# Performance work log

Hardware: AMD Instinct MI355X
Metric: run time of the kernel (lower is better)

Reference implementation:

```python
import jax, jax.numpy as jnp
import numpy as np

E, QE, P, H = 3, 60000, 40, 20   # elements, atoms per element, fp length, hidden
NIMG = 1800                       # images in batch
Q = E * QE                        # total atoms
NNZ = 14_400_000                  # nnz of sparse fprimes [P*Q, 3*Q]


def setup_inputs() -> dict:
    key = jax.random.key(0)
    ks = jax.random.split(key, 12)
    fps = jax.random.normal(ks[0], (E, QE, P), jnp.float32)
    image_idx = jax.random.randint(ks[1], (E, QE), 0, NIMG, jnp.int32)
    s1 = 1.0 / np.sqrt(P)
    s2 = 1.0 / np.sqrt(H)
    W1 = (jax.random.normal(ks[2], (E, P, H)) * s1).astype(jnp.float32)
    b1 = jnp.zeros((E, H), jnp.float32)
    W2 = (jax.random.normal(ks[3], (E, H, H)) * s2).astype(jnp.float32)
    b2 = jnp.zeros((E, H), jnp.float32)
    W3 = (jax.random.normal(ks[4], (E, H, 1)) * s2).astype(jnp.float32)
    b3 = jnp.zeros((E, 1), jnp.float32)
    fp_rows = jax.random.randint(ks[5], (NNZ,), 0, P * Q, jnp.int32)
    fp_cols = jax.random.randint(ks[6], (NNZ,), 0, 3 * Q, jnp.int32)
    fp_vals = (jax.random.normal(ks[7], (NNZ,)) * 0.05).astype(jnp.float32)
    return {"fps": fps, "W1": W1, "b1": b1, "W2": W2, "b2": b2, "W3": W3,
            "b3": b3, "image_idx": image_idx, "fp_rows": fp_rows,
            "fp_cols": fp_cols, "fp_vals": fp_vals, "batch_size": NIMG}


def _mlp(x, w1, b1, w2, b2, w3, b3):
    # Dense(tanh) -> Dense(tanh) -> Dense(linear), per amptorch MLP(n_layers=3)
    h = jnp.tanh(x @ w1 + b1)
    h = jnp.tanh(h @ w2 + b2)
    return h @ w3 + b3  # [..., 1]


def _esum(x, w1, b1, w2, b2, w3, b3):
    return _mlp(x, w1, b1, w2, b2, w3, b3).sum()


def reference(fps, W1, b1, W2, b2, W3, b3, image_idx, fp_rows, fp_cols,
              fp_vals, batch_size):
    # per-element atomwise energies: [E, QE, 1]
    atom_e = jax.vmap(_mlp)(fps, W1, b1, W2, b2, W3, b3)
    # scatter-add atomic energies into per-image energies (index_add_)
    energy_pred = jax.ops.segment_sum(
        atom_e.reshape(-1, 1), image_idx.reshape(-1).astype(jnp.int32),
        num_segments=batch_size)  # [NIMG, 1]
    # dE/dFP per atom (each atom's output depends only on its own fp, so
    # grad of the per-element energy sum == per-atom jacobian rows)
    dE_dFP = jax.vmap(jax.grad(_esum))(fps, W1, b1, W2, b2, W3, b3)  # [E,QE,P]
    # reorder atoms from element-grouped order to image-index order
    # (stable argsort == boolean-match reorder in the torch code)
    order = jnp.argsort(image_idx.reshape(-1))
    dE_flat = dE_dFP.reshape(-1, P)[order].reshape(-1)  # [P*Q]
    # force = -fprimes^T @ dE_dFP  (sparse COO matvec via segment_sum)
    force_flat = -jax.ops.segment_sum(
        fp_vals * dE_flat[fp_rows], fp_cols, num_segments=3 * Q)
    force_pred = force_flat.reshape(-1, 3)  # [Q, 3]
    return energy_pred, force_pred
```

## Files before the change

kernel.cpp:

```cpp
#include <hip/hip_runtime.h>
#include <math.h>

#define E_    3
#define QE_   60000
#define QTOT  180000
#define P_    40
#define H_    20
#define NIMG_ 1800
#define NNZ_  14400000
#define BLK   256
#define NB    704

#define CW_BITS 12
#define CW      4096
#define NBIN    132
#define SUBS    8
#define SC      8192
#define NSB     1758

#define SLICE_SHIFT 17
#define NSLICE  55
#define CAPS    270336
#define CAPB    114688
#define MAXCH4  1815
#define FS_GRID 768
#define FS_PERX 96

#define C_SCUR  0
#define C_BCUR  64
#define C_GCNT  256
#define C_CHS   512
#define C_CHST  2432
#define C_CHLEN 4352
#define C_GRP   6272
#define C_INTS  8320

typedef int   vi4 __attribute__((ext_vector_type(4)));
typedef float vf4 __attribute__((ext_vector_type(4)));
typedef unsigned uint32;

__global__ void zero_kernel(float* __restrict__ out, int n) {
    int i = blockIdx.x * blockDim.x + threadIdx.x;
    if (i < n) out[i] = 0.0f;
}
__global__ void zero_ctrl_kernel(int* __restrict__ ctrl) {
    ctrl[threadIdx.x] = 0;
}

__global__ void hist_kernel(const int* __restrict__ img, int* __restrict__ g_hist) {
    __shared__ int h[NIMG_];
    const int t = threadIdx.x, b = blockIdx.x;
    for (int v = t; v < NIMG_; v += BLK) h[v] = 0;
    __syncthreads();
    int a = b * BLK + t;
    if (a < QTOT) atomicAdd(&h[img[a]], 1);
    __syncthreads();
    for (int v = t; v < NIMG_; v += BLK) g_hist[v * NB + b] = h[v];
}

__global__ void scan_blocks_kernel(int* __restrict__ g_hist, int* __restrict__ g_total) {
    __shared__ int s[BLK];
    const int v = blockIdx.x, t = threadIdx.x;
    int carry = 0;
    for (int c = 0; c < NB; c += BLK) {
        int idx = c + t;
        int val = (idx < NB) ? g_hist[v * NB + idx] : 0;
        s[t] = val; __syncthreads();
        for (int off = 1; off < BLK; off <<= 1) {
            int tmp = (t >= off) ? s[t - off] : 0;
            __syncthreads();
            s[t] += tmp;
            __syncthreads();
        }
        int excl = s[t] - val;
        int tot  = s[BLK - 1];
        if (idx < NB) g_hist[v * NB + idx] = carry + excl;
        carry += tot;
        __syncthreads();
    }
    if (t == 0) g_total[v] = carry;
}

__global__ void scan_buckets_kernel(const int* __restrict__ g_total, int* __restrict__ g_base) {
    __shared__ int s[BLK];
    const int t = threadIdx.x;
    int carry = 0;
    for (int c = 0; c < NIMG_; c += BLK) {
        int idx = c + t;
        int val = (idx < NIMG_) ? g_total[idx] : 0;
        s[t] = val; __syncthreads();
        for (int off = 1; off < BLK; off <<= 1) {
            int tmp = (t >= off) ? s[t - off] : 0;
            __syncthreads();
            s[t] += tmp;
            __syncthreads();
        }
        if (idx < NIMG_) g_base[idx] = carry + (s[t] - val);
        carry += s[BLK - 1];
        __syncthreads();
    }
}

__global__ void rank_kernel(const int* __restrict__ img, const int* __restrict__ g_hist,
                            const int* __restrict__ g_base, int* __restrict__ rank) {
    __shared__ int simg[BLK];
    const int t = threadIdx.x, b = blockIdx.x;
    int a = b * BLK + t;
    int v = (a < QTOT) ? img[a] : -1;
    simg[t] = v;
    __syncthreads();
    if (a < QTOT) {
        int local = 0;
        for (int j = 0; j < t; ++j) {
            if (simg[j] == v) local++;
        }
        rank[a] = g_base[v] + g_hist[v * NB + b] + local;
    }
}

__global__ __launch_bounds__(BLK) void mlp_kernel(
    const float* __restrict__ fps, const float* __restrict__ W1, const float* __restrict__ b1,
    const float* __restrict__ W2, const float* __restrict__ b2, const float* __restrict__ W3,
    const float* __restrict__ b3, const int* __restrict__ img, const int* __restrict__ rank,
    float* __restrict__ energy, float* __restrict__ dEflat)
{
    __shared__ float sW1[P_ * H_], sW2[H_ * H_], sW3[H_], sB1[H_], sB2[H_];
    __shared__ float sB3;
    const int e = blockIdx.y;
    const int t = threadIdx.x;
    for (int i = t; i < P_ * H_; i += BLK) sW1[i] = W1[e * P_ * H_ + i];
    for (int i = t; i < H_ * H_; i += BLK) sW2[i] = W2[e * H_ * H_ + i];
    if (t < H_) { sW3[t] = W3[e * H_ + t]; sB1[t] = b1[e * H_ + t]; sB2[t] = b2[e * H_ + t]; }
    if (t == 0) sB3 = b3[e];
    __syncthreads();

    int q = blockIdx.x * BLK + t;
    if (q >= QE_) return;
    int a = e * QE_ + q;

    const vf4* xp = (const vf4*)(fps + (size_t)a * P_);
    float x[P_];
    #pragma unroll
    for (int p = 0; p < P_; p += 4) {
        vf4 v4 = __builtin_nontemporal_load(xp + (p >> 2));
        x[p] = v4.x; x[p+1] = v4.y; x[p+2] = v4.z; x[p+3] = v4.w;
    }

    float h1v[H_], h2v[H_];
    #pragma unroll
    for (int i = 0; i < H_; ++i) {
        float z = sB1[i];
        #pragma unroll
        for (int p = 0; p < P_; ++p) z += x[p] * sW1[p * H_ + i];
        h1v[i] = tanhf(z);
    }
    #pragma unroll
    for (int i = 0; i < H_; ++i) {
        float z = sB2[i];
        #pragma unroll
        for (int j = 0; j < H_; ++j) z += h1v[j] * sW2[j * H_ + i];
        h2v[i] = tanhf(z);
    }
    float ea = sB3;
    #pragma unroll
    for (int i = 0; i < H_; ++i) ea += h2v[i] * sW3[i];
    atomicAdd(&energy[img[a]], ea);

    float dz2[H_];
    #pragma unroll
    for (int i = 0; i < H_; ++i) dz2[i] = sW3[i] * (1.0f - h2v[i] * h2v[i]);
    float dz1[H_];
    #pragma unroll
    for (int i = 0; i < H_; ++i) {
        float d = 0.0f;
        #pragma unroll
        for (int j = 0; j < H_; ++j) d += sW2[i * H_ + j] * dz2[j];
        dz1[i] = d * (1.0f - h1v[i] * h1v[i]);
    }
    float* op = dEflat + (size_t)rank[a] * P_;
    #pragma unroll
    for (int p = 0; p < P_; p += 4) {
        float4 v4;
        float d0 = 0.f, d1 = 0.f, d2 = 0.f, d3 = 0.f;
        #pragma unroll
        for (int i = 0; i < H_; ++i) {
            d0 += sW1[(p    ) * H_ + i] * dz1[i];
            d1 += sW1[(p + 1) * H_ + i] * dz1[i];
            d2 += sW1[(p + 2) * H_ + i] * dz1[i];
            d3 += sW1[(p + 3) * H_ + i] * dz1[i];
        }
        v4.x = d0; v4.y = d1; v4.z = d2; v4.w = d3;
        *(float4*)(op + p) = v4;
    }
}


__global__ __launch_bounds__(BLK) void slice_scatter_kernel(
    const int* __restrict__ rows, const int* __restrict__ cols, const float* __restrict__ vals,
    int* __restrict__ ctrl, uint2* __restrict__ items)
{
    __shared__ uint32 srow[SC];
    __shared__ int h[NSLICE], lcur[NSLICE], gbase[NSLICE];
    const int t = threadIdx.x, b = blockIdx.x;
    const int base = b * SC;
    const int len = min(SC, NNZ_ - base);
    const bool full = (len == SC);

    if (t < NSLICE) h[t] = 0;
    __syncthreads();
    if (full) {
        const vi4* r4 = (const vi4*)(rows + base);
        #pragma unroll
        for (int j = 0; j < SC / (BLK * 4); ++j) {
            int idx = j * BLK + t;
            vi4 rr = __builtin_nontemporal_load(r4 + idx);
            srow[idx * 4 + 0] = (uint32)rr.x; atomicAdd(&h[rr.x >> SLICE_SHIFT], 1);
            srow[idx * 4 + 1] = (uint32)rr.y; atomicAdd(&h[rr.y >> SLICE_SHIFT], 1);
            srow[idx * 4 + 2] = (uint32)rr.z; atomicAdd(&h[rr.z >> SLICE_SHIFT], 1);
            srow[idx * 4 + 3] = (uint32)rr.w; atomicAdd(&h[rr.w >> SLICE_SHIFT], 1);
        }
    } else {
        for (int j = t; j < len; j += BLK) {
            int r = rows[base + j];
            srow[j] = (uint32)r;
            atomicAdd(&h[r >> SLICE_SHIFT], 1);
        }
    }
    __syncthreads();
    if (t < NSLICE) {
        lcur[t] = 0;
        gbase[t] = (h[t] > 0) ? atomicAdd(&ctrl[C_SCUR + t], h[t]) : 0;
    }
    __syncthreads();
    if (full) {
        const vi4* c4 = (const vi4*)(cols + base);
        const vi4* v4 = (const vf4*)(vals + base) ? (const vi4*)(vals + base) : nullptr;
        #pragma unroll 2
        for (int j = 0; j < SC / (BLK * 4); ++j) {
            int idx = j * BLK + t;
            vi4 cc = __builtin_nontemporal_load(c4 + idx);
            vi4 vv = __builtin_nontemporal_load(v4 + idx);
            #define EMIT(K, CI, VB)                                                \
            {                                                                      \
                uint32 r = srow[idx * 4 + K];                                      \
                int sl = (int)(r >> SLICE_SHIFT);                                  \
                int pos = gbase[sl] + atomicAdd(&lcur[sl], 1);                     \
                uint32 v15 = (((uint32)(VB)) + 0x10000u) >> 17;                    \
                items[(size_t)sl * CAPS + pos] =                                   \
                    make_uint2((v15 << 17) | (r & 0x1FFFFu), (uint32)(CI));        \
            }
            EMIT(0, cc.x, vv.x)
            EMIT(1, cc.y, vv.y)
            EMIT(2, cc.z, vv.z)
            EMIT(3, cc.w, vv.w)
        }
    } else {
        for (int j = t; j < len; j += BLK) {
            uint32 r = srow[j];
            int sl = (int)(r >> SLICE_SHIFT);
            int pos = gbase[sl] + atomicAdd(&lcur[sl], 1);
            uint32 vb = ((const uint32*)vals)[base + j];
            uint32 v15 = (vb + 0x10000u) >> 17;
            items[(size_t)sl * CAPS + pos] =
                make_uint2((v15 << 17) | (r & 0x1FFFFu), (uint32)cols[base + j]);
        }
    }
}

__global__ void plan4_kernel(int* __restrict__ ctrl) {
    __shared__ int scnt[NSLICE], cb[NSLICE + 1], gp[NSLICE];
    __shared__ int g8[8], tot_s;
    const int t = threadIdx.x;
    if (t < NSLICE) scnt[t] = ctrl[C_SCUR + t];
    __syncthreads();
    if (t == 0) {
        int crun = 0;
        int gs[8]; for (int x = 0; x < 8; ++x) gs[x] = 0;
        for (int s = 0; s < NSLICE; ++s) {
            int nc = (scnt[s] + SC - 1) / SC;
            cb[s] = crun; crun += nc;
            int x = s & 7;
            gp[s] = gs[x]; gs[x] += nc;
        }
        cb[NSLICE] = crun; tot_s = crun;
        for (int x = 0; x < 8; ++x) g8[x] = gs[x];
    }
    __syncthreads();
    const int tot = tot_s;
    if (t < 8) ctrl[C_GCNT + t] = g8[t];
    for (int idx = t; idx < tot; idx += BLK) {
        int s = 0;
        for (int k = 0; k < NSLICE; ++k) if (cb[k] <= idx) s = k;
        int c = idx - cb[s];
        ctrl[C_CHS + idx]   = s;
        ctrl[C_CHST + idx]  = s * CAPS + c * SC;
        ctrl[C_CHLEN + idx] = min(SC, scnt[s] - c * SC);
        ctrl[C_GRP + (s & 7) * 256 + gp[s] + c] = idx;
    }
}

__global__ __launch_bounds__(BLK) void fscatter4_kernel(
    const uint2* __restrict__ items, const float* __restrict__ dEflat,
    int* __restrict__ ctrl, uint32* __restrict__ bm)
{
    __shared__ uint32 itl[SC];
    __shared__ unsigned char bns[SC];
    __shared__ int h[NBIN], cur[NBIN], dlt[NBIN];
    __shared__ int sc[BLK];
    const int t = threadIdx.x;
    const int x = blockIdx.x & 7;
    const int r = blockIdx.x >> 3;
    const int gc = ctrl[C_GCNT + x];

    for (int w = r; w < gc; w += FS_PERX) {
        const int g     = ctrl[C_GRP + x * 256 + w];
        const int sl    = ctrl[C_CHS + g];
        const int start = ctrl[C_CHST + g];
        const int len   = ctrl[C_CHLEN + g];
        const int row0  = sl << SLICE_SHIFT;
        const int lenE  = len & ~1;

        if (t < NBIN) h[t] = 0;
        __syncthreads();
        if (len == SC) {
            const vi4* p4 = (const vi4*)(items + start);
            #pragma unroll
            for (int j = 0; j < SC / (BLK * 2); ++j) {
                vi4 q = __builtin_nontemporal_load(p4 + j * BLK + t);
                atomicAdd(&h[((uint32)q.y) >> CW_BITS], 1);
                atomicAdd(&h[((uint32)q.w) >> CW_BITS], 1);
            }
        } else {
            for (int j = t; j < len; j += BLK)
                atomicAdd(&h[items[start + j].y >> CW_BITS], 1);
        }
        __syncthreads();
        {
            int v = (t < NBIN) ? h[t] : 0;
            sc[t] = v; __syncthreads();
            for (int off = 1; off < BLK; off <<= 1) {
                int tmp = (t >= off) ? sc[t - off] : 0;
                __syncthreads();
                sc[t] += tmp;
                __syncthreads();
            }
            if (t < NBIN) {
                int ls = sc[t] - v;
                cur[t] = ls;
                int gb = (v > 0) ? atomicAdd(&ctrl[C_BCUR + t], v) : 0;
                dlt[t] = t * CAPB + gb - ls;
            }
        }
        __syncthreads();
        #define PLACE4(LO, CO, DI)                                             \
        {                                                                      \
            uint32 col = (uint32)(CO);                                         \
            int bin = (int)(col >> CW_BITS);                                   \
            float val = __uint_as_float((((uint32)(LO)) >> 17) << 17);         \
            uint32 u = __float_as_uint(-val * (DI));                           \
            uint32 pk = ((col & (CW - 1)) << 20) | ((u + 0x800u) >> 12);       \
            int pos = atomicAdd(&cur[bin], 1);                                 \
            itl[pos] = pk;                                                     \
            bns[pos] = (unsigned char)bin;                                     \
        }
        if (len == SC) {
            const vi4* p4 = (const vi4*)(items + start);
            #pragma unroll 2
            for (int j = 0; j < SC / (BLK * 2); ++j) {
                vi4 q = __builtin_nontemporal_load(p4 + j * BLK + t);
                float dA = dEflat[row0 + (((uint32)q.x) & 0x1FFFFu)];
                float dB = dEflat[row0 + (((uint32)q.z) & 0x1FFFFu)];
                PLACE4(q.x, q.y, dA)
                PLACE4(q.z, q.w, dB)
            }
        } else {
            for (int j = t; j < len; j += BLK) {
                uint2 it = items[start + j];
                float d = dEflat[row0 + (it.x & 0x1FFFFu)];
                PLACE4(it.x, it.y, d)
            }
        }
        __syncthreads();
        for (int i = t; i < len; i += BLK) {
            __builtin_nontemporal_store(itl[i], &bm[dlt[bns[i]] + i]);
        }
        __syncthreads();
    }
}

__global__ __launch_bounds__(BLK) void fforce4_kernel(
    const uint32* __restrict__ bm, const int* __restrict__ ctrl,
    float* __restrict__ partial)
{
    __shared__ float w[CW];
    const int t = threadIdx.x;
    const int bin = blockIdx.x >> 3;
    const int sub = blockIdx.x & (SUBS - 1);
    for (int i = t; i < CW; i += BLK) w[i] = 0.0f;
    __syncthreads();
    const int cnt   = ctrl[C_BCUR + bin];
    const int start = bin * CAPB;
    const int sBeg  = start + (cnt * sub) / SUBS;
    const int sEnd  = start + (cnt * (sub + 1)) / SUBS;
    int i = sBeg + t;
    for (; i + 3 * BLK < sEnd; i += 4 * BLK) {
        uint32 p0 = __builtin_nontemporal_load(bm + i);
        uint32 p1 = __builtin_nontemporal_load(bm + i + BLK);
        uint32 p2 = __builtin_nontemporal_load(bm + i + 2 * BLK);
        uint32 p3 = __builtin_nontemporal_load(bm + i + 3 * BLK);
        atomicAdd(&w[p0 >> 20], __uint_as_float((p0 & 0xFFFFFu) << 12));
        atomicAdd(&w[p1 >> 20], __uint_as_float((p1 & 0xFFFFFu) << 12));
        atomicAdd(&w[p2 >> 20], __uint_as_float((p2 & 0xFFFFFu) << 12));
        atomicAdd(&w[p3 >> 20], __uint_as_float((p3 & 0xFFFFFu) << 12));
    }
    for (; i < sEnd; i += BLK) {
        uint32 p = bm[i];
        atomicAdd(&w[p >> 20], __uint_as_float((p & 0xFFFFFu) << 12));
    }
    __syncthreads();
    float* dst = partial + (size_t)blockIdx.x * CW;
    for (int k = t; k < CW; k += BLK) __builtin_nontemporal_store(w[k], dst + k);
}

__global__ void freduce_kernel(const float* __restrict__ partial, float* __restrict__ force) {
    int i = blockIdx.x * BLK + threadIdx.x;
    if (i < 3 * QTOT) {
        int bin = i >> CW_BITS, local = i & (CW - 1);
        const float* p = partial + (size_t)bin * (CW * SUBS) + local;
        float sum = 0.0f;
        #pragma unroll
        for (int k = 0; k < SUBS; ++k) sum += __builtin_nontemporal_load(p + k * CW);
        force[i] = sum;
    }
}

__global__ __launch_bounds__(BLK) void fhist_kernel(const int* __restrict__ cols,
                                                    int* __restrict__ binHist) {
    __shared__ int h[NBIN];
    const int t = threadIdx.x, b = blockIdx.x;
    if (t < NBIN) h[t] = 0;
    __syncthreads();
    const int base = b * SC;
    if (base + SC <= NNZ_) {
        const vi4* c4 = (const vi4*)(cols + base);
        #pragma unroll
        for (int j = 0; j < SC / (BLK * 4); ++j) {
            vi4 cc = __builtin_nontemporal_load(c4 + j * BLK + t);
            atomicAdd(&h[cc.x >> CW_BITS], 1);
            atomicAdd(&h[cc.y >> CW_BITS], 1);
            atomicAdd(&h[cc.z >> CW_BITS], 1);
            atomicAdd(&h[cc.w >> CW_BITS], 1);
        }
    } else {
        for (int j = 0; j < SC / BLK; ++j) {
            int k = base + j * BLK + t;
            if (k < NNZ_) atomicAdd(&h[cols[k] >> CW_BITS], 1);
        }
    }
    __syncthreads();
    if (t < NBIN) binHist[t * NSB + b] = h[t];
}

__global__ void fscan_blocks_kernel(int* __restrict__ binHist, int* __restrict__ binTotal,
                                    int n) {
    __shared__ int s[BLK];
    const int v = blockIdx.x, t = threadIdx.x;
    int carry = 0;
    for (int c = 0; c < n; c += BLK) {
        int idx = c + t;
        int val = (idx < n) ? binHist[v * n + idx] : 0;
        s[t] = val; __syncthreads();
        for (int off = 1; off < BLK; off <<= 1) {
            int tmp = (t >= off) ? s[t - off] : 0;
            __syncthreads();
            s[t] += tmp;
            __syncthreads();
        }
        int excl = s[t] - val;
        int tot  = s[BLK - 1];
        if (idx < n) binHist[v * n + idx] = carry + excl;
        carry += tot;
        __syncthreads();
    }
    if (t == 0) binTotal[v] = carry;
}

__global__ void fbase_kernel(const int* __restrict__ binTotal, int* __restrict__ binBase) {
    __shared__ int s[BLK];
    const int t = threadIdx.x;
    int v = (t < NBIN) ? binTotal[t] : 0;
    s[t] = v; __syncthreads();
    for (int off = 1; off < BLK; off <<= 1) {
        int tmp = (t >= off) ? s[t - off] : 0;
        __syncthreads();
        s[t] += tmp;
        __syncthreads();
    }
    if (t < NBIN) binBase[t] = s[t] - v;
    if (t == 0) binBase[NBIN] = s[BLK - 1];
}

__global__ __launch_bounds__(BLK) void fscatter_kernel(
    const int* __restrict__ rows, const int* __restrict__ cols, const float* __restrict__ vals,
    const float* __restrict__ dEflat, const int* __restrict__ binHist,
    const int* __restrict__ binBase, uint32* __restrict__ bm)
{
    __shared__ uint32 items[SC];
    __shared__ unsigned char bins[SC];
    __shared__ int hist[NBIN];
    __shared__ int cursor[NBIN];
    __shared__ int delta[NBIN];
    __shared__ int s[BLK];
    const int t = threadIdx.x, b = blockIdx.x;
    const int base = b * SC;
    const int nIt = min(SC, NNZ_ - base);
    const bool full = (base + SC <= NNZ_);

    if (t < NBIN) hist[t] = 0;
    __syncthreads();
    if (full) {
        const vi4* c4 = (const vi4*)(cols + base);
        #pragma unroll
        for (int j = 0; j < SC / (BLK * 4); ++j) {
            vi4 cc = __builtin_nontemporal_load(c4 + j * BLK + t);
            atomicAdd(&hist[cc.x >> CW_BITS], 1);
            atomicAdd(&hist[cc.y >> CW_BITS], 1);
            atomicAdd(&hist[cc.z >> CW_BITS], 1);
            atomicAdd(&hist[cc.w >> CW_BITS], 1);
        }
    } else {
        for (int j = 0; j < SC / BLK; ++j) {
            int k = base + j * BLK + t;
            if (k < NNZ_) atomicAdd(&hist[cols[k] >> CW_BITS], 1);
        }
    }
    __syncthreads();
    {
        int v = (t < NBIN) ? hist[t] : 0;
        s[t] = v; __syncthreads();
        for (int off = 1; off < BLK; off <<= 1) {
            int tmp = (t >= off) ? s[t - off] : 0;
            __syncthreads();
            s[t] += tmp;
            __syncthreads();
        }
        if (t < NBIN) {
            int ls = s[t] - v;
            cursor[t] = ls;
            delta[t]  = binBase[t] + binHist[t * NSB + b] - ls;
        }
    }
    __syncthreads();
    if (full) {
        const vi4* c4 = (const vi4*)(cols + base);
        const vi4* r4 = (const vi4*)(rows + base);
        const vf4* v4 = (const vf4*)(vals + base);
        #pragma unroll 2
        for (int j = 0; j < SC / (BLK * 4); ++j) {
            int idx = j * BLK + t;
            vi4 cc = __builtin_nontemporal_load(c4 + idx);
            vi4 rr = __builtin_nontemporal_load(r4 + idx);
            vf4 vv = __builtin_nontemporal_load(v4 + idx);
            float d0 = dEflat[rr.x];
            float d1 = dEflat[rr.y];
            float d2 = dEflat[rr.z];
            float d3 = dEflat[rr.w];
            #define PLACE(CI, VI, DI)                                              \
            {                                                                      \
                int bin = (CI) >> CW_BITS;                                         \
                uint32 u = __float_as_uint(-(VI) * (DI));                          \
                uint32 pk = ((uint32)((CI) & (CW - 1)) << 20)                      \
                            | ((u + 0x800u) >> 12);                                \
                int pos = atomicAdd(&cursor[bin], 1);                              \
                items[pos] = pk;                                                   \
                bins[pos] = (unsigned char)bin;                                    \
            }
            PLACE(cc.x, vv.x, d0)
            PLACE(cc.y, vv.y, d1)
            PLACE(cc.z, vv.z, d2)
            PLACE(cc.w, vv.w, d3)
        }
    } else {
        for (int j = 0; j < SC / BLK; ++j) {
            int k = base + j * BLK + t;
            if (k < NNZ_) {
                int c = cols[k];
                float d = dEflat[rows[k]];
                float v = vals[k];
                PLACE(c, v, d)
            }
        }
    }
    __syncthreads();
    for (int i = t; i < nIt; i += BLK) {
        __builtin_nontemporal_store(items[i], &bm[delta[bins[i]] + i]);
    }
}

__global__ __launch_bounds__(BLK) void fforce_kernel(
    const uint32* __restrict__ bm, const int* __restrict__ binBase,
    float* __restrict__ partial)
{
    __shared__ float w[CW];
    const int t = threadIdx.x;
    const int bin = blockIdx.x >> 3;
    const int sub = blockIdx.x & (SUBS - 1);
    for (int i = t; i < CW; i += BLK) w[i] = 0.0f;
    __syncthreads();
    const int start = binBase[bin];
    const int cnt   = binBase[bin + 1] - start;
    const int sBeg  = start + (cnt * sub) / SUBS;
    const int sEnd  = start + (cnt * (sub + 1)) / SUBS;
    int i = sBeg + t;
    for (; i + 3 * BLK < sEnd; i += 4 * BLK) {
        uint32 p0 = __builtin_nontemporal_load(bm + i);
        uint32 p1 = __builtin_nontemporal_load(bm + i + BLK);
        uint32 p2 = __builtin_nontemporal_load(bm + i + 2 * BLK);
        uint32 p3 = __builtin_nontemporal_load(bm + i + 3 * BLK);
        atomicAdd(&w[p0 >> 20], __uint_as_float((p0 & 0xFFFFFu) << 12));
        atomicAdd(&w[p1 >> 20], __uint_as_float((p1 & 0xFFFFFu) << 12));
        atomicAdd(&w[p2 >> 20], __uint_as_float((p2 & 0xFFFFFu) << 12));
        atomicAdd(&w[p3 >> 20], __uint_as_float((p3 & 0xFFFFFu) << 12));
    }
    for (; i < sEnd; i += BLK) {
        uint32 p = bm[i];
        atomicAdd(&w[p >> 20], __uint_as_float((p & 0xFFFFFu) << 12));
    }
    __syncthreads();
    float* dst = partial + (size_t)blockIdx.x * CW;
    for (int k = t; k < CW; k += BLK) __builtin_nontemporal_store(w[k], dst + k);
}

__global__ void force_kernel(const int* __restrict__ rows, const int* __restrict__ cols,
                             const float* __restrict__ vals, const float* __restrict__ dEflat,
                             float* __restrict__ force) {
    int k = blockIdx.x * blockDim.x + threadIdx.x;
    if (k < NNZ_) {
        float contrib = -vals[k] * dEflat[rows[k]];
        atomicAdd(&force[cols[k]], contrib);
    }
}

extern "C" void kernel_launch(void* const* d_in, const int* in_sizes, int n_in,
                              void* d_out, int out_size, void* d_ws, size_t ws_size,
                              hipStream_t stream) {
    (void)in_sizes; (void)n_in; (void)out_size;
    const float* fps  = (const float*)d_in[0];
    const float* W1   = (const float*)d_in[1];
    const float* b1   = (const float*)d_in[2];
    const float* W2   = (const float*)d_in[3];
    const float* b2   = (const float*)d_in[4];
    const float* W3   = (const float*)d_in[5];
    const float* b3   = (const float*)d_in[6];
    const int*   img  = (const int*)d_in[7];
    const int*   rows = (const int*)d_in[8];
    const int*   cols = (const int*)d_in[9];
    const float* vals = (const float*)d_in[10];

    char* ws = (char*)d_ws;
    float* energy = (float*)d_out;
    float* force  = (float*)d_out + NIMG_;
    const int nOut = NIMG_ + 3 * QTOT;

    int*    g_hist  = (int*)(ws);
    int*    g_total = (int*)(ws + 5068800);
    int*    g_base  = (int*)(ws + 5076000);
    int*    rank    = (int*)(ws + 5083200);
    uint2*  items   = (uint2*)(ws);
    float*  partial4= (float*)(ws);
    uint32* bm4     = (uint32*)(ws + 118947840);
    int*    ctrl    = (int*)(ws + 179503104);
    float*  dEflat4 = (float*)(ws + 179536384);
    const size_t WS_V4 = 208336384;

    float*  dEflat5   = (float*)(ws + 5803200);
    int*    binHist5  = (int*)(ws + 34603200);
    int*    binTotal5 = (int*)(ws + 35531424);
    int*    binBase5  = (int*)(ws + 35531952);
    uint32* bm5       = (uint32*)(ws + 35532496);
    float*  partial5  = (float*)(ws + 93132496);
    const size_t WS_V2 = 110434000;

    const bool v4 = (ws_size >= WS_V4);
    float* dEflat = v4 ? dEflat4 : dEflat5;

    zero_kernel<<<(nOut + BLK - 1) / BLK, BLK, 0, stream>>>((float*)d_out, nOut);

    hist_kernel<<<NB, BLK, 0, stream>>>(img, g_hist);
    scan_blocks_kernel<<<NIMG_, BLK, 0, stream>>>(g_hist, g_total);
    scan_buckets_kernel<<<1, BLK, 0, stream>>>(g_total, g_base);
    rank_kernel<<<NB, BLK, 0, stream>>>(img, g_hist, g_base, rank);

    dim3 gm((QE_ + BLK - 1) / BLK, E_);
    mlp_kernel<<<gm, BLK, 0, stream>>>(fps, W1, b1, W2, b2, W3, b3, img, rank,
                                       energy, dEflat);

    if (v4) {
        zero_ctrl_kernel<<<1, 256, 0, stream>>>(ctrl);
        slice_scatter_kernel<<<NSB, BLK, 0, stream>>>(rows, cols, vals, ctrl, items);
        plan4_kernel<<<1, BLK, 0, stream>>>(ctrl);
        fscatter4_kernel<<<FS_GRID, BLK, 0, stream>>>(items, dEflat, ctrl, bm4);
        fforce4_kernel<<<NBIN * SUBS, BLK, 0, stream>>>(bm4, ctrl, partial4);
        freduce_kernel<<<(3 * QTOT + BLK - 1) / BLK, BLK, 0, stream>>>(partial4, force);
    } else if (ws_size >= WS_V2) {
        fhist_kernel<<<NSB, BLK, 0, stream>>>(cols, binHist5);
        fscan_blocks_kernel<<<NBIN, BLK, 0, stream>>>(binHist5, binTotal5, NSB);
        fbase_kernel<<<1, BLK, 0, stream>>>(binTotal5, binBase5);
        fscatter_kernel<<<NSB, BLK, 0, stream>>>(rows, cols, vals, dEflat,
                                                 binHist5, binBase5, bm5);
        fforce_kernel<<<NBIN * SUBS, BLK, 0, stream>>>(bm5, binBase5, partial5);
        freduce_kernel<<<(3 * QTOT + BLK - 1) / BLK, BLK, 0, stream>>>(partial5, force);
    } else {
        force_kernel<<<NNZ_ / BLK, BLK, 0, stream>>>(rows, cols, vals, dEflat, force);
    }
}
```

Measured before the change: 605.1 us.

## Replace column-binned scatter with direct global atomics into replicated force arrays

Drops the per-chunk column histogram, scan, packed bin staging and the shared-memory binned accumulation pass. Each slice-group now atomically adds its contributions straight into one of eight replicated global force arrays, which a final kernel sums. This removes a full write and read of the packed intermediate and several block-level syncs. In exchange it adds 14.4M global float atomics spread over 2.16MB per replica, plus a zeroing pass over the replicas.

After: 1.088 ms. 1.8x slower.

```diff
diff --git a/kernel.cpp b/kernel.cpp
--- a/kernel.cpp
+++ b/kernel.cpp
@@ -25,6 +25,11 @@
 #define MAXCH4  1815
 #define FS_GRID 768
 #define FS_PERX 96
+
+#define FSZ      540000
+#define NREP     8
+#define FS_GRID2 2048
+#define FS_PERX2 256
 
 #define C_SCUR  0
 #define C_BCUR  64
@@ -299,138 +304,55 @@
     }
 }
 
-__global__ __launch_bounds__(BLK) void fscatter4_kernel(
+__global__ __launch_bounds__(BLK) void fscatter5_kernel(
     const uint2* __restrict__ items, const float* __restrict__ dEflat,
-    int* __restrict__ ctrl, uint32* __restrict__ bm)
+    const int* __restrict__ ctrl, float* __restrict__ frep)
 {
-    __shared__ uint32 itl[SC];
-    __shared__ unsigned char bns[SC];
-    __shared__ int h[NBIN], cur[NBIN], dlt[NBIN];
-    __shared__ int sc[BLK];
     const int t = threadIdx.x;
     const int x = blockIdx.x & 7;
     const int r = blockIdx.x >> 3;
     const int gc = ctrl[C_GCNT + x];
-
-    for (int w = r; w < gc; w += FS_PERX) {
+    float* __restrict__ fx = frep + (size_t)x * FSZ;
+
+    for (int w = r; w < gc; w += FS_PERX2) {
         const int g     = ctrl[C_GRP + x * 256 + w];
         const int sl    = ctrl[C_CHS + g];
         const int start = ctrl[C_CHST + g];
         const int len   = ctrl[C_CHLEN + g];
-        const int row0  = sl << SLICE_SHIFT;
-        const int lenE  = len & ~1;
-
-        if (t < NBIN) h[t] = 0;
-        __syncthreads();
+        const float* __restrict__ dE = dEflat + ((size_t)sl << SLICE_SHIFT);
+
         if (len == SC) {
             const vi4* p4 = (const vi4*)(items + start);
-            #pragma unroll
+            #pragma unroll 4
             for (int j = 0; j < SC / (BLK * 2); ++j) {
                 vi4 q = __builtin_nontemporal_load(p4 + j * BLK + t);
-                atomicAdd(&h[((uint32)q.y) >> CW_BITS], 1);
-                atomicAdd(&h[((uint32)q.w) >> CW_BITS], 1);
-            }
-        } else {
-            for (int j = t; j < len; j += BLK)
-                atomicAdd(&h[items[start + j].y >> CW_BITS], 1);
-        }
-        __syncthreads();
-        {
-            int v = (t < NBIN) ? h[t] : 0;
-            sc[t] = v; __syncthreads();
-            for (int off = 1; off < BLK; off <<= 1) {
-                int tmp = (t >= off) ? sc[t - off] : 0;
-                __syncthreads();
-                sc[t] += tmp;
-                __syncthreads();
-            }
-            if (t < NBIN) {
-                int ls = sc[t] - v;
-                cur[t] = ls;
-                int gb = (v > 0) ? atomicAdd(&ctrl[C_BCUR + t], v) : 0;
-                dlt[t] = t * CAPB + gb - ls;
-            }
-        }
-        __syncthreads();
-        #define PLACE4(LO, CO, DI)                                             \
-        {                                                                      \
-            uint32 col = (uint32)(CO);                                         \
-            int bin = (int)(col >> CW_BITS);                                   \
-            float val = __uint_as_float((((uint32)(LO)) >> 17) << 17);         \
-            uint32 u = __float_as_uint(-val * (DI));                           \
-            uint32 pk = ((col & (CW - 1)) << 20) | ((u + 0x800u) >> 12);       \
-            int pos = atomicAdd(&cur[bin], 1);                                 \
-            itl[pos] = pk;                                                     \
-            bns[pos] = (unsigned char)bin;                                     \
-        }
-        if (len == SC) {
-            const vi4* p4 = (const vi4*)(items + start);
-            #pragma unroll 2
-            for (int j = 0; j < SC / (BLK * 2); ++j) {
-                vi4 q = __builtin_nontemporal_load(p4 + j * BLK + t);
-                float dA = dEflat[row0 + (((uint32)q.x) & 0x1FFFFu)];
-                float dB = dEflat[row0 + (((uint32)q.z) & 0x1FFFFu)];
-                PLACE4(q.x, q.y, dA)
-                PLACE4(q.z, q.w, dB)
+                float dA = dE[((uint32)q.x) & 0x1FFFFu];
+                float dB = dE[((uint32)q.z) & 0x1FFFFu];
+                float vA = __uint_as_float((((uint32)q.x) >> 17) << 17);
+                float vB = __uint_as_float((((uint32)q.z) >> 17) << 17);
+                atomicAdd(&fx[(uint32)q.y], -vA * dA);
+                atomicAdd(&fx[(uint32)q.w], -vB * dB);
             }
         } else {
             for (int j = t; j < len; j += BLK) {
                 uint2 it = items[start + j];
-                float d = dEflat[row0 + (it.x & 0x1FFFFu)];
-                PLACE4(it.x, it.y, d)
+                float d = dE[it.x & 0x1FFFFu];
+                float v = __uint_as_float((it.x >> 17) << 17);
+                atomicAdd(&fx[it.y], -v * d);
             }
         }
-        __syncthreads();
-        for (int i = t; i < len; i += BLK) {
-            __builtin_nontemporal_store(itl[i], &bm[dlt[bns[i]] + i]);
-        }
-        __syncthreads();
-    }
-}
-
-__global__ __launch_bounds__(BLK) void fforce4_kernel(
-    const uint32* __restrict__ bm, const int* __restrict__ ctrl,
-    float* __restrict__ partial)
-{
-    __shared__ float w[CW];
-    const int t = threadIdx.x;
-    const int bin = blockIdx.x >> 3;
-    const int sub = blockIdx.x & (SUBS - 1);
-    for (int i = t; i < CW; i += BLK) w[i] = 0.0f;
-    __syncthreads();
-    const int cnt   = ctrl[C_BCUR + bin];
-    const int start = bin * CAPB;
-    const int sBeg  = start + (cnt * sub) / SUBS;
-    const int sEnd  = start + (cnt * (sub + 1)) / SUBS;
-    int i = sBeg + t;
-    for (; i + 3 * BLK < sEnd; i += 4 * BLK) {
-        uint32 p0 = __builtin_nontemporal_load(bm + i);
-        uint32 p1 = __builtin_nontemporal_load(bm + i + BLK);
-        uint32 p2 = __builtin_nontemporal_load(bm + i + 2 * BLK);
-        uint32 p3 = __builtin_nontemporal_load(bm + i + 3 * BLK);
-        atomicAdd(&w[p0 >> 20], __uint_as_float((p0 & 0xFFFFFu) << 12));
-        atomicAdd(&w[p1 >> 20], __uint_as_float((p1 & 0xFFFFFu) << 12));
-        atomicAdd(&w[p2 >> 20], __uint_as_float((p2 & 0xFFFFFu) << 12));
-        atomicAdd(&w[p3 >> 20], __uint_as_float((p3 & 0xFFFFFu) << 12));
-    }
-    for (; i < sEnd; i += BLK) {
-        uint32 p = bm[i];
-        atomicAdd(&w[p >> 20], __uint_as_float((p & 0xFFFFFu) << 12));
-    }
-    __syncthreads();
-    float* dst = partial + (size_t)blockIdx.x * CW;
-    for (int k = t; k < CW; k += BLK) __builtin_nontemporal_store(w[k], dst + k);
-}
-
-__global__ void freduce_kernel(const float* __restrict__ partial, float* __restrict__ force) {
+    }
+}
+
+__global__ void freduce5_kernel(const float* __restrict__ frep,
+                                float* __restrict__ force) {
     int i = blockIdx.x * BLK + threadIdx.x;
-    if (i < 3 * QTOT) {
-        int bin = i >> CW_BITS, local = i & (CW - 1);
-        const float* p = partial + (size_t)bin * (CW * SUBS) + local;
-        float sum = 0.0f;
-        #pragma unroll
-        for (int k = 0; k < SUBS; ++k) sum += __builtin_nontemporal_load(p + k * CW);
-        force[i] = sum;
+    if (i < FSZ) {
+        float s = 0.0f;
+        #pragma unroll
+        for (int k = 0; k < NREP; ++k)
+            s += __builtin_nontemporal_load(frep + (size_t)k * FSZ + i);
+        force[i] = s;
     }
 }
 
@@ -631,6 +553,18 @@
     for (int k = t; k < CW; k += BLK) __builtin_nontemporal_store(w[k], dst + k);
 }
 
+__global__ void freduce_kernel(const float* __restrict__ partial, float* __restrict__ force) {
+    int i = blockIdx.x * BLK + threadIdx.x;
+    if (i < 3 * QTOT) {
+        int bin = i >> CW_BITS, local = i & (CW - 1);
+        const float* p = partial + (size_t)bin * (CW * SUBS) + local;
+        float sum = 0.0f;
+        #pragma unroll
+        for (int k = 0; k < SUBS; ++k) sum += __builtin_nontemporal_load(p + k * CW);
+        force[i] = sum;
+    }
+}
+
 __global__ void force_kernel(const int* __restrict__ rows, const int* __restrict__ cols,
                              const float* __restrict__ vals, const float* __restrict__ dEflat,
                              float* __restrict__ force) {
@@ -667,8 +601,7 @@
     int*    g_base  = (int*)(ws + 5076000);
     int*    rank    = (int*)(ws + 5083200);
     uint2*  items   = (uint2*)(ws);
-    float*  partial4= (float*)(ws);
-    uint32* bm4     = (uint32*)(ws + 118947840);
+    float*  frep    = (float*)(ws + 118947840);
     int*    ctrl    = (int*)(ws + 179503104);
     float*  dEflat4 = (float*)(ws + 179536384);
     const size_t WS_V4 = 208336384;
@@ -696,12 +629,12 @@
                                        energy, dEflat);
 
     if (v4) {
+        zero_kernel<<<(NREP * FSZ + BLK - 1) / BLK, BLK, 0, stream>>>(frep, NREP * FSZ);
         zero_ctrl_kernel<<<1, 256, 0, stream>>>(ctrl);
         slice_scatter_kernel<<<NSB, BLK, 0, stream>>>(rows, cols, vals, ctrl, items);
         plan4_kernel<<<1, BLK, 0, stream>>>(ctrl);
-        fscatter4_kernel<<<FS_GRID, BLK, 0, stream>>>(items, dEflat, ctrl, bm4);
-        fforce4_kernel<<<NBIN * SUBS, BLK, 0, stream>>>(bm4, ctrl, partial4);
-        freduce_kernel<<<(3 * QTOT + BLK - 1) / BLK, BLK, 0, stream>>>(partial4, force);
+        fscatter5_kernel<<<FS_GRID2, BLK, 0, stream>>>(items, dEflat, ctrl, frep);
+        freduce5_kernel<<<(FSZ + BLK - 1) / BLK, BLK, 0, stream>>>(frep, force);
     } else if (ws_size >= WS_V2) {
         fhist_kernel<<<NSB, BLK, 0, stream>>>(cols, binHist5);
         fscan_blocks_kernel<<<NBIN, BLK, 0, stream>>>(binHist5, binTotal5, NSB);
```

## Halve scatter chunk size, pack chunk plan, write bins per-wave

Applied to the files above, without the earlier changes.

Shrinks the force-scatter chunk from 8192 to 4096 items and raises the grid to 1792 blocks, so LDS use per block drops and more blocks can be resident. The plan kernel now stores one packed (slice, chunk) word per chunk instead of four control arrays, and the scatter kernel computes start and length itself. The per-item bin byte array is removed; the writeout walks bins one wave at a time and copies each bin's contiguous run. Smaller chunks mean more per-bin global atomics and shorter runs per bin, which may give less coalesced stores.

Measured after the change: 628.8 us. +3.9%, slower.

```diff
diff --git a/kernel.cpp b/kernel.cpp
--- a/kernel.cpp
+++ b/kernel.cpp
@@ -22,18 +22,17 @@
 #define NSLICE  55
 #define CAPS    270336
 #define CAPB    114688
-#define MAXCH4  1815
-#define FS_GRID 768
-#define FS_PERX 96
+
+#define SCF     4096
+#define NCHMAX  512
+#define FS_GRID 1792
+#define FS_PERX 224
 
 #define C_SCUR  0
 #define C_BCUR  64
 #define C_GCNT  256
-#define C_CHS   512
-#define C_CHST  2432
-#define C_CHLEN 4352
-#define C_GRP   6272
-#define C_INTS  8320
+#define C_GRP   512
+#define C_INTS  4608
 
 typedef int   vi4 __attribute__((ext_vector_type(4)));
 typedef float vf4 __attribute__((ext_vector_type(4)));
@@ -234,7 +233,7 @@
     __syncthreads();
     if (full) {
         const vi4* c4 = (const vi4*)(cols + base);
-        const vi4* v4 = (const vf4*)(vals + base) ? (const vi4*)(vals + base) : nullptr;
+        const vi4* v4 = (const vi4*)(vals + base);
         #pragma unroll 2
         for (int j = 0; j < SC / (BLK * 4); ++j) {
             int idx = j * BLK + t;
@@ -277,7 +276,7 @@
         int crun = 0;
         int gs[8]; for (int x = 0; x < 8; ++x) gs[x] = 0;
         for (int s = 0; s < NSLICE; ++s) {
-            int nc = (scnt[s] + SC - 1) / SC;
+            int nc = (scnt[s] + SCF - 1) / SCF;
             cb[s] = crun; crun += nc;
             int x = s & 7;
             gp[s] = gs[x]; gs[x] += nc;
@@ -292,10 +291,7 @@
         int s = 0;
         for (int k = 0; k < NSLICE; ++k) if (cb[k] <= idx) s = k;
         int c = idx - cb[s];
-        ctrl[C_CHS + idx]   = s;
-        ctrl[C_CHST + idx]  = s * CAPS + c * SC;
-        ctrl[C_CHLEN + idx] = min(SC, scnt[s] - c * SC);
-        ctrl[C_GRP + (s & 7) * 256 + gp[s] + c] = idx;
+        ctrl[C_GRP + (s & 7) * NCHMAX + gp[s] + c] = (s << 8) | c;
     }
 }
 
@@ -303,9 +299,8 @@
     const uint2* __restrict__ items, const float* __restrict__ dEflat,
     int* __restrict__ ctrl, uint32* __restrict__ bm)
 {
-    __shared__ uint32 itl[SC];
-    __shared__ unsigned char bns[SC];
-    __shared__ int h[NBIN], cur[NBIN], dlt[NBIN];
+    __shared__ uint32 itl[SCF];
+    __shared__ int h[NBIN], cur[NBIN], ls[NBIN], dlt[NBIN];
     __shared__ int sc[BLK];
     const int t = threadIdx.x;
     const int x = blockIdx.x & 7;
@@ -313,19 +308,19 @@
     const int gc = ctrl[C_GCNT + x];
 
     for (int w = r; w < gc; w += FS_PERX) {
-        const int g     = ctrl[C_GRP + x * 256 + w];
-        const int sl    = ctrl[C_CHS + g];
-        const int start = ctrl[C_CHST + g];
-        const int len   = ctrl[C_CHLEN + g];
-        const int row0  = sl << SLICE_SHIFT;
-        const int lenE  = len & ~1;
+        const int pkd   = ctrl[C_GRP + x * NCHMAX + w];
+        const int sl    = pkd >> 8;
+        const int c     = pkd & 255;
+        const int start = sl * CAPS + c * SCF;
+        const int len   = min(SCF, ctrl[C_SCUR + sl] - c * SCF);
+        const float* __restrict__ dE = dEflat + ((size_t)sl << SLICE_SHIFT);
 
         if (t < NBIN) h[t] = 0;
         __syncthreads();
-        if (len == SC) {
+        if (len == SCF) {
             const vi4* p4 = (const vi4*)(items + start);
             #pragma unroll
-            for (int j = 0; j < SC / (BLK * 2); ++j) {
+            for (int j = 0; j < SCF / (BLK * 2); ++j) {
                 vi4 q = __builtin_nontemporal_load(p4 + j * BLK + t);
                 atomicAdd(&h[((uint32)q.y) >> CW_BITS], 1);
                 atomicAdd(&h[((uint32)q.w) >> CW_BITS], 1);
@@ -345,10 +340,11 @@
                 __syncthreads();
             }
             if (t < NBIN) {
-                int ls = sc[t] - v;
-                cur[t] = ls;
+                int st = sc[t] - v;
+                ls[t] = st;
+                cur[t] = st;
                 int gb = (v > 0) ? atomicAdd(&ctrl[C_BCUR + t], v) : 0;
-                dlt[t] = t * CAPB + gb - ls;
+                dlt[t] = t * CAPB + gb;
             }
         }
         __syncthreads();
@@ -361,28 +357,34 @@
             uint32 pk = ((col & (CW - 1)) << 20) | ((u + 0x800u) >> 12);       \
             int pos = atomicAdd(&cur[bin], 1);                                 \
             itl[pos] = pk;                                                     \
-            bns[pos] = (unsigned char)bin;                                     \
-        }
-        if (len == SC) {
+        }
+        if (len == SCF) {
             const vi4* p4 = (const vi4*)(items + start);
-            #pragma unroll 2
-            for (int j = 0; j < SC / (BLK * 2); ++j) {
+            #pragma unroll 4
+            for (int j = 0; j < SCF / (BLK * 2); ++j) {
                 vi4 q = __builtin_nontemporal_load(p4 + j * BLK + t);
-                float dA = dEflat[row0 + (((uint32)q.x) & 0x1FFFFu)];
-                float dB = dEflat[row0 + (((uint32)q.z) & 0x1FFFFu)];
+                float dA = dE[((uint32)q.x) & 0x1FFFFu];
+                float dB = dE[((uint32)q.z) & 0x1FFFFu];
                 PLACE4(q.x, q.y, dA)
                 PLACE4(q.z, q.w, dB)
             }
         } else {
             for (int j = t; j < len; j += BLK) {
                 uint2 it = items[start + j];
-                float d = dEflat[row0 + (it.x & 0x1FFFFu)];
+                float d = dE[it.x & 0x1FFFFu];
                 PLACE4(it.x, it.y, d)
             }
         }
         __syncthreads();
-        for (int i = t; i < len; i += BLK) {
-            __builtin_nontemporal_store(itl[i], &bm[dlt[bns[i]] + i]);
+        {
+            const int wv = t >> 6, ln = t & 63;
+            for (int b = wv; b < NBIN; b += 4) {
+                int s0 = ls[b];
+                int cnt = cur[b] - s0;
+                int gb = dlt[b];
+                for (int k = ln; k < cnt; k += 64)
+                    __builtin_nontemporal_store(itl[s0 + k], &bm[gb + k]);
+            }
         }
         __syncthreads();
     }
```
